# Performance work log

Measured on AMD Instinct MI355X. Metric: run time of the kernel, lower is better.

The kernel has to match this reference:

```python
import jax, jax.numpy as jnp
import numpy as np

N_NODES = 100000
N_EDGES = 1250000
HID = 64
IN_CH = 64
OUT_CH = 16
N_GRAPHS = 512


def setup_inputs() -> dict:
    key = jax.random.key(0)
    ks = jax.random.split(key, 20)
    x = jax.random.normal(ks[0], (N_NODES, IN_CH), dtype=jnp.float32)
    edge_index = jax.random.randint(ks[1], (2, N_EDGES), 0, N_NODES, dtype=jnp.int64)
    batch = jnp.sort(jax.random.randint(ks[2], (N_NODES,), 0, N_GRAPHS, dtype=jnp.int64))
    s_in = 1.0 / np.sqrt(IN_CH)
    s_h = 1.0 / np.sqrt(HID)
    u = lambda k, shp, s: jax.random.uniform(k, shp, jnp.float32, -s, s)
    return {
        "x": x, "edge_index": edge_index, "batch": batch,
        "W0": u(ks[3], (IN_CH, HID), s_in), "b0": u(ks[4], (HID,), s_in),
        "W1a": u(ks[5], (HID, HID), s_h), "b1a": u(ks[6], (HID,), s_h),
        "W1b": u(ks[7], (HID, HID), s_h), "b1b": u(ks[8], (HID,), s_h),
        "W2a": u(ks[9], (HID, HID), s_h), "b2a": u(ks[10], (HID,), s_h),
        "W2b": u(ks[11], (HID, HID), s_h), "b2b": u(ks[12], (HID,), s_h),
        "W3a": u(ks[13], (HID, HID), s_h), "b3a": u(ks[14], (HID,), s_h),
        "W3b": u(ks[15], (HID, HID), s_h), "b3b": u(ks[16], (HID,), s_h),
        "Wl": u(ks[17], (HID, OUT_CH), s_h), "bl": u(ks[18], (OUT_CH,), s_h),
    }


def _gin_conv(h, src, dst, Wa, ba, Wb, bb):
    # GINConv, eps=0: mlp(x_i + sum_{j->i} x_j); mlp = Linear,ReLU,Linear
    agg = jax.ops.segment_sum(h[src], dst, num_segments=N_NODES)  # [N, HID]
    z = h + agg
    return jax.nn.relu(z @ Wa + ba) @ Wb + bb


def reference(x, edge_index, batch, W0, b0, W1a, b1a, W1b, b1b,
              W2a, b2a, W2b, b2b, W3a, b3a, W3b, b3b, Wl, bl):
    src, dst = edge_index[0], edge_index[1]
    h = jax.nn.relu(x @ W0 + b0)
    h = jax.nn.relu(_gin_conv(h, src, dst, W1a, b1a, W1b, b1b))
    h = jax.nn.relu(_gin_conv(h, src, dst, W2a, b2a, W2b, b2b))
    h = jax.nn.relu(_gin_conv(h, src, dst, W3a, b3a, W3b, b3b))
    # global mean pool over graphs
    sums = jax.ops.segment_sum(h, batch, num_segments=N_GRAPHS)  # [G, HID]
    cnts = jax.ops.segment_sum(jnp.ones((N_NODES,), h.dtype), batch, num_segments=N_GRAPHS)
    pooled = sums / jnp.maximum(cnts, 1.0)[:, None]
    # dropout p=0.5 is identity in eval mode
    return pooled @ Wl + bl  # [G, OUT_CH]
```

## Files before the change

### kernel.cpp

```cpp
#include <hip/hip_runtime.h>
#include <hip/hip_fp16.h>

#define N_NODES 100000
#define N_EDGES 1250000
#define HID 64
#define N_GRAPHS 512
#define OUT_CH 16

#define NSUP 196
#define SB_CAP 8192
#define E_BLK 2048
#define NPB ((N_EDGES + E_BLK - 1) / E_BLK)
#define TILE2 ((N_NODES + 127) / 128)
#define NWP 6
#define TSTRIDE 68
#define AGG_BLOCKS 3125

typedef _Float16 h16;
typedef _Float16 half2_t __attribute__((ext_vector_type(2)));
typedef _Float16 f16x8 __attribute__((ext_vector_type(8)));
typedef float f32x4 __attribute__((ext_vector_type(4)));

__device__ __forceinline__ void acc4(uint2 u, float& a0, float& a1, float& a2, float& a3) {
    half2_t h0 = __builtin_bit_cast(half2_t, u.x);
    half2_t h1 = __builtin_bit_cast(half2_t, u.y);
    a0 += (float)h0[0];
    a1 += (float)h0[1];
    a2 += (float)h1[0];
    a3 += (float)h1[1];
}

__device__ __forceinline__ void acc8(uint4 u, float* a) {
    half2_t h0 = __builtin_bit_cast(half2_t, u.x);
    half2_t h1 = __builtin_bit_cast(half2_t, u.y);
    half2_t h2 = __builtin_bit_cast(half2_t, u.z);
    half2_t h3 = __builtin_bit_cast(half2_t, u.w);
    a[0] += (float)h0[0]; a[1] += (float)h0[1];
    a[2] += (float)h1[0]; a[3] += (float)h1[1];
    a[4] += (float)h2[0]; a[5] += (float)h2[1];
    a[6] += (float)h3[0]; a[7] += (float)h3[1];
}

__device__ __forceinline__ unsigned pack2(float x, float y) {
    half2_t o;
    o[0] = (h16)x;
    o[1] = (h16)y;
    return __builtin_bit_cast(unsigned, o);
}

__global__ __launch_bounds__(256) void k_fat(const int* __restrict__ src,
                                             const int* __restrict__ dst,
                                             int* __restrict__ cnt,
                                             int* __restrict__ buckets,
                                             const float* __restrict__ W1a,
                                             const float* __restrict__ W1b,
                                             const float* __restrict__ W2a,
                                             const float* __restrict__ W2b,
                                             const float* __restrict__ W3a,
                                             const float* __restrict__ W3b,
                                             h16* __restrict__ WF,
                                             const float* __restrict__ W0,
                                             const float* __restrict__ B0,
                                             const float* __restrict__ Xin,
                                             h16* __restrict__ Hout) {
    __shared__ int hist[256];
    __shared__ int gbase[256];
    __shared__ int tsum[256];
    __shared__ __align__(16) int stage[E_BLK];
    __shared__ __align__(16) float sT[4 * 16 * TSTRIDE];

    int b = blockIdx.x;
    int t = threadIdx.x;

    if (b < NPB) {
        int e0 = b * E_BLK;
        int eN = N_EDGES - e0;
        if (eN > E_BLK) eN = E_BLK;

        hist[t] = 0;
        __syncthreads();
        for (int i = t; i < eN; i += 256) atomicAdd(&hist[dst[e0 + i] >> 9], 1);
        __syncthreads();

        int c = hist[t];
        tsum[t] = c;
        __syncthreads();
        for (int off = 1; off < 256; off <<= 1) {
            int u = (t >= off) ? tsum[t - off] : 0;
            __syncthreads();
            tsum[t] += u;
            __syncthreads();
        }
        int pref = tsum[t] - c;
        if (t < NSUP && c > 0) gbase[t] = atomicAdd(&cnt[t], c);
        hist[t] = pref;
        __syncthreads();

        for (int i = t; i < eN; i += 256) {
            int s = src[e0 + i];
            int d = dst[e0 + i];
            int p = atomicAdd(&hist[d >> 9], 1);
            stage[p] = ((d & 511) << 17) | s;
        }
        __syncthreads();

        if (t < NSUP && c > 0) {
            int lstart = hist[t] - c;
            int gb = gbase[t];
            int cap = SB_CAP - gb;
            int n = c < cap ? c : (cap > 0 ? cap : 0);
            int* dp = buckets + (size_t)t * SB_CAP + gb;
            int r = 0;
            while (r < n && (((size_t)(dp + r)) & 15)) { dp[r] = stage[lstart + r]; ++r; }
            for (; r + 4 <= n; r += 4) {
                int4 v;
                v.x = stage[lstart + r];
                v.y = stage[lstart + r + 1];
                v.z = stage[lstart + r + 2];
                v.w = stage[lstart + r + 3];
                *(int4*)(dp + r) = v;
            }
            for (; r < n; ++r) dp[r] = stage[lstart + r];
        }
    } else if (b < NPB + NWP) {
        const float* Ws[NWP] = {W1a, W1b, W2a, W2b, W3a, W3b};
        const float* W = Ws[b - NPB];
        h16* dstW = WF + (size_t)(b - NPB) * 4096;
#pragma unroll
        for (int i = 0; i < 16; ++i) {
            int s = t + 256 * i;
            int k = s >> 6, col = s & 63;
            int kc = k >> 5, quad = (k >> 3) & 3, j = k & 7;
            int c = col >> 4, n = col & 15;
            dstW[((c * 2 + kc) * 4 + quad) * 128 + n * 8 + j] = (h16)W[s];
        }
    } else {
        int lb = b - NPB - NWP;
        int w = t >> 6, lane = t & 63;
        int n16 = lane & 15, quad = lane >> 4;
        float* T = sT + w * 16 * TSTRIDE;

        f16x8 bw[4][2];
#pragma unroll
        for (int c = 0; c < 4; ++c)
#pragma unroll
            for (int kc = 0; kc < 2; ++kc) {
                f16x8 v;
#pragma unroll
                for (int j = 0; j < 8; ++j)
                    v[j] = (h16)W0[(kc * 32 + quad * 8 + j) * 64 + c * 16 + n16];
                bw[c][kc] = v;
            }
        float bv[4];
#pragma unroll
        for (int c = 0; c < 4; ++c) bv[c] = B0[c * 16 + n16];

#pragma unroll
        for (int tt = 0; tt < 2; ++tt) {
            int rbase = lb * 128 + tt * 64 + w * 16;
            int arow = rbase + n16;
            int crow = arow < N_NODES ? arow : N_NODES - 1;
            f16x8 a[2];
#pragma unroll
            for (int kc = 0; kc < 2; ++kc) {
                const float4* xp = (const float4*)(Xin + (size_t)crow * HID + kc * 32 + quad * 8);
                float4 p = xp[0], q = xp[1];
                f16x8 v;
                v[0] = (h16)p.x; v[1] = (h16)p.y; v[2] = (h16)p.z; v[3] = (h16)p.w;
                v[4] = (h16)q.x; v[5] = (h16)q.y; v[6] = (h16)q.z; v[7] = (h16)q.w;
                a[kc] = v;
            }

            f32x4 acc[4];
#pragma unroll
            for (int c = 0; c < 4; ++c) {
                acc[c] = (f32x4){bv[c], bv[c], bv[c], bv[c]};
#pragma unroll
                for (int kc = 0; kc < 2; ++kc)
                    acc[c] = __builtin_amdgcn_mfma_f32_16x16x32_f16(a[kc], bw[c][kc], acc[c], 0, 0, 0);
            }

#pragma unroll
            for (int c = 0; c < 4; ++c)
#pragma unroll
                for (int r = 0; r < 4; ++r)
                    T[(quad * 4 + r) * TSTRIDE + c * 16 + n16] = fmaxf(acc[c][r], 0.f);
            {
                int rl = lane >> 2, seg = lane & 3;
                int row = rbase + rl;
                if (row < N_NODES) {
                    const float* tr = &T[rl * TSTRIDE + seg * 16];
                    f16x8 o0, o1;
#pragma unroll
                    for (int i = 0; i < 8; ++i) {
                        o0[i] = (h16)tr[i];
                        o1[i] = (h16)tr[8 + i];
                    }
                    f16x8* dp = (f16x8*)(Hout + (size_t)row * HID + seg * 16);
                    dp[0] = o0;
                    dp[1] = o1;
                }
            }
        }
    }
}

__global__ __launch_bounds__(256) void k_sort(const int* __restrict__ cnt,
                                              int* __restrict__ buckets,
                                              int* __restrict__ rowptrS) {
    __shared__ int srt[SB_CAP];
    __shared__ int hist[512];
    __shared__ int curs[512];
    __shared__ int tsum[256];
    int s = blockIdx.x, t = threadIdx.x;
    int n = cnt[s];
    n = n < SB_CAP ? n : SB_CAP;
    int* gb = buckets + (size_t)s * SB_CAP;
    int sBase = s * SB_CAP;

    hist[t] = 0;
    hist[t + 256] = 0;
    __syncthreads();
    for (int i = t; i < n; i += 256) atomicAdd(&hist[gb[i] >> 17], 1);
    __syncthreads();

    int c0 = hist[2 * t], c1 = hist[2 * t + 1];
    int tot = c0 + c1;
    tsum[t] = tot;
    __syncthreads();
    for (int off = 1; off < 256; off <<= 1) {
        int u = (t >= off) ? tsum[t - off] : 0;
        __syncthreads();
        tsum[t] += u;
        __syncthreads();
    }
    int pref = tsum[t] - tot;
    curs[2 * t] = pref;
    curs[2 * t + 1] = pref + c0;
    rowptrS[s * 513 + 2 * t] = sBase + pref;
    rowptrS[s * 513 + 2 * t + 1] = sBase + pref + c0;
    if (t == 255) rowptrS[s * 513 + 512] = sBase + n;
    __syncthreads();

    for (int i = t; i < n; i += 256) {
        int rec = gb[i];
        int pos = atomicAdd(&curs[rec >> 17], 1);
        srt[pos] = rec;
    }
    __syncthreads();
    for (int i = t; i < n; i += 256) gb[i] = srt[i];
}

__global__ __launch_bounds__(256) void k_aggregate(const int* __restrict__ rowptrS,
                                                   const int* __restrict__ buckets,
                                                   const h16* __restrict__ H,
                                                   h16* __restrict__ Z) {
    const uint4* H8 = (const uint4*)H;
    uint4* Z8 = (uint4*)Z;
    int lane = threadIdx.x & 63;
    int part = lane >> 3, sub = lane & 7;
    int gwave = (blockIdx.x * 256 + threadIdx.x) >> 6;
    int nw = (gridDim.x * 256) >> 6;
    for (int i0 = gwave * 8; i0 < N_NODES; i0 += nw * 8) {
        int i = i0 + part;
        bool valid = i < N_NODES;
        int iv = valid ? i : N_NODES - 1;
        int s = iv >> 9, l = iv & 511;
        int start = rowptrS[s * 513 + l];
        int end = valid ? rowptrS[s * 513 + l + 1] : start;
        float a[8] = {0.f, 0.f, 0.f, 0.f, 0.f, 0.f, 0.f, 0.f};
        acc8(H8[(size_t)iv * 8 + sub], a);
        int j = start;
        for (; j + 8 <= end; j += 8) {
            int s0 = buckets[j] & 0x1FFFF;
            int s1 = buckets[j + 1] & 0x1FFFF;
            int s2 = buckets[j + 2] & 0x1FFFF;
            int s3 = buckets[j + 3] & 0x1FFFF;
            int s4 = buckets[j + 4] & 0x1FFFF;
            int s5 = buckets[j + 5] & 0x1FFFF;
            int s6 = buckets[j + 6] & 0x1FFFF;
            int s7 = buckets[j + 7] & 0x1FFFF;
            uint4 u0 = H8[(size_t)s0 * 8 + sub];
            uint4 u1 = H8[(size_t)s1 * 8 + sub];
            uint4 u2 = H8[(size_t)s2 * 8 + sub];
            uint4 u3 = H8[(size_t)s3 * 8 + sub];
            uint4 u4 = H8[(size_t)s4 * 8 + sub];
            uint4 u5 = H8[(size_t)s5 * 8 + sub];
            uint4 u6 = H8[(size_t)s6 * 8 + sub];
            uint4 u7 = H8[(size_t)s7 * 8 + sub];
            acc8(u0, a);
            acc8(u1, a);
            acc8(u2, a);
            acc8(u3, a);
            acc8(u4, a);
            acc8(u5, a);
            acc8(u6, a);
            acc8(u7, a);
        }
        if (j + 4 <= end) {
            int s0 = buckets[j] & 0x1FFFF;
            int s1 = buckets[j + 1] & 0x1FFFF;
            int s2 = buckets[j + 2] & 0x1FFFF;
            int s3 = buckets[j + 3] & 0x1FFFF;
            uint4 u0 = H8[(size_t)s0 * 8 + sub];
            uint4 u1 = H8[(size_t)s1 * 8 + sub];
            uint4 u2 = H8[(size_t)s2 * 8 + sub];
            uint4 u3 = H8[(size_t)s3 * 8 + sub];
            acc8(u0, a);
            acc8(u1, a);
            acc8(u2, a);
            acc8(u3, a);
            j += 4;
        }
        if (j + 2 <= end) {
            int s0 = buckets[j] & 0x1FFFF;
            int s1 = buckets[j + 1] & 0x1FFFF;
            uint4 u0 = H8[(size_t)s0 * 8 + sub];
            uint4 u1 = H8[(size_t)s1 * 8 + sub];
            acc8(u0, a);
            acc8(u1, a);
            j += 2;
        }
        if (j < end) {
            int s0 = buckets[j] & 0x1FFFF;
            acc8(H8[(size_t)s0 * 8 + sub], a);
        }
        if (valid) {
            uint4 o;
            o.x = pack2(a[0], a[1]);
            o.y = pack2(a[2], a[3]);
            o.z = pack2(a[4], a[5]);
            o.w = pack2(a[6], a[7]);
            Z8[(size_t)i * 8 + sub] = o;
        }
    }
}

__global__ __launch_bounds__(256) void k_mlp(const h16* __restrict__ WaF,
                                             const float* __restrict__ Ba,
                                             const h16* __restrict__ WbF,
                                             const float* __restrict__ Bb,
                                             const h16* __restrict__ Zin,
                                             h16* __restrict__ Hout) {
    __shared__ __align__(16) float sT[4 * 16 * TSTRIDE];
    int t = threadIdx.x;
    int w = t >> 6, lane = t & 63;
    int n16 = lane & 15, quad = lane >> 4;
    float* T = sT + w * 16 * TSTRIDE;

    f16x8 bwa[4][2], bwb[4][2];
#pragma unroll
    for (int c = 0; c < 4; ++c)
#pragma unroll
        for (int kc = 0; kc < 2; ++kc) {
            int f = ((c * 2 + kc) * 4 + quad) * 128 + n16 * 8;
            bwa[c][kc] = *(const f16x8*)(WaF + f);
            bwb[c][kc] = *(const f16x8*)(WbF + f);
        }
    float bva[4], bvb[4];
#pragma unroll
    for (int c = 0; c < 4; ++c) {
        bva[c] = Ba[c * 16 + n16];
        bvb[c] = Bb[c * 16 + n16];
    }

#pragma unroll
    for (int tt = 0; tt < 2; ++tt) {
        int rbase = blockIdx.x * 128 + tt * 64 + w * 16;
        int arow = rbase + n16;
        int crow = arow < N_NODES ? arow : N_NODES - 1;
        const f16x8* zp = (const f16x8*)(Zin + (size_t)crow * HID + quad * 8);
        f16x8 a0 = zp[0];
        f16x8 a1 = zp[4];

        f32x4 acc[4];
#pragma unroll
        for (int c = 0; c < 4; ++c) {
            acc[c] = (f32x4){bva[c], bva[c], bva[c], bva[c]};
            acc[c] = __builtin_amdgcn_mfma_f32_16x16x32_f16(a0, bwa[c][0], acc[c], 0, 0, 0);
            acc[c] = __builtin_amdgcn_mfma_f32_16x16x32_f16(a1, bwa[c][1], acc[c], 0, 0, 0);
        }

#pragma unroll
        for (int c = 0; c < 4; ++c)
#pragma unroll
            for (int r = 0; r < 4; ++r)
                T[(quad * 4 + r) * TSTRIDE + c * 16 + n16] = fmaxf(acc[c][r], 0.f);

        f16x8 ta[2];
#pragma unroll
        for (int kc = 0; kc < 2; ++kc) {
            float4 p = *(const float4*)&T[n16 * TSTRIDE + kc * 32 + quad * 8];
            float4 q = *(const float4*)&T[n16 * TSTRIDE + kc * 32 + quad * 8 + 4];
            f16x8 v;
            v[0] = (h16)p.x; v[1] = (h16)p.y; v[2] = (h16)p.z; v[3] = (h16)p.w;
            v[4] = (h16)q.x; v[5] = (h16)q.y; v[6] = (h16)q.z; v[7] = (h16)q.w;
            ta[kc] = v;
        }

#pragma unroll
        for (int c = 0; c < 4; ++c) {
            acc[c] = (f32x4){bvb[c], bvb[c], bvb[c], bvb[c]};
            acc[c] = __builtin_amdgcn_mfma_f32_16x16x32_f16(ta[0], bwb[c][0], acc[c], 0, 0, 0);
            acc[c] = __builtin_amdgcn_mfma_f32_16x16x32_f16(ta[1], bwb[c][1], acc[c], 0, 0, 0);
        }

#pragma unroll
        for (int c = 0; c < 4; ++c)
#pragma unroll
            for (int r = 0; r < 4; ++r)
                T[(quad * 4 + r) * TSTRIDE + c * 16 + n16] = fmaxf(acc[c][r], 0.f);
        {
            int rl = lane >> 2, seg = lane & 3;
            int row = rbase + rl;
            if (row < N_NODES) {
                const float* tr = &T[rl * TSTRIDE + seg * 16];
                f16x8 o0, o1;
#pragma unroll
                for (int i = 0; i < 8; ++i) {
                    o0[i] = (h16)tr[i];
                    o1[i] = (h16)tr[8 + i];
                }
                f16x8* dp = (f16x8*)(Hout + (size_t)row * HID + seg * 16);
                dp[0] = o0;
                dp[1] = o1;
            }
        }
    }
}

__global__ __launch_bounds__(256) void k_poolfinal(const h16* __restrict__ H,
                                                   const int* __restrict__ batch,
                                                   const float* __restrict__ Wl,
                                                   const float* __restrict__ bl,
                                                   float* __restrict__ out) {
    __shared__ float sp[4 * HID];
    int g = blockIdx.x;
    int t = threadIdx.x;
    int lane = t & 63, w = t >> 6;
    int lo = 0, hi = N_NODES;
    while (lo < hi) { int m = (lo + hi) >> 1; if (batch[m] < g) lo = m + 1; else hi = m; }
    int start = lo;
    hi = N_NODES;
    while (lo < hi) { int m = (lo + hi) >> 1; if (batch[m] < g + 1) lo = m + 1; else hi = m; }
    int end = lo;
    float s0 = 0.f, s1 = 0.f, s2 = 0.f, s3 = 0.f;
    int r = start + w;
    for (; r + 12 < end; r += 16) {
        float v0 = (float)H[(size_t)r * HID + lane];
        float v1 = (float)H[(size_t)(r + 4) * HID + lane];
        float v2 = (float)H[(size_t)(r + 8) * HID + lane];
        float v3 = (float)H[(size_t)(r + 12) * HID + lane];
        s0 += v0; s1 += v1; s2 += v2; s3 += v3;
    }
    for (; r < end; r += 4) s0 += (float)H[(size_t)r * HID + lane];
    sp[w * HID + lane] = s0 + s1 + s2 + s3;
    __syncthreads();
    if (t < HID) {
        float tot = sp[t] + sp[HID + t] + sp[2 * HID + t] + sp[3 * HID + t];
        float c = (end > start) ? (float)(end - start) : 1.0f;
        sp[t] = tot / c;
    }
    __syncthreads();
    if (t < OUT_CH) {
        float acc = bl[t];
#pragma unroll
        for (int k = 0; k < HID; ++k) acc += sp[k] * Wl[k * OUT_CH + t];
        out[g * OUT_CH + t] = acc;
    }
}

extern "C" void kernel_launch(void* const* d_in, const int* in_sizes, int n_in,
                              void* d_out, int out_size, void* d_ws, size_t ws_size,
                              hipStream_t stream) {
    const float* x     = (const float*)d_in[0];
    const int*   edge  = (const int*)d_in[1];
    const int*   batch = (const int*)d_in[2];
    const float* W0  = (const float*)d_in[3];
    const float* b0  = (const float*)d_in[4];
    const float* W1a = (const float*)d_in[5];
    const float* b1a = (const float*)d_in[6];
    const float* W1b = (const float*)d_in[7];
    const float* b1b = (const float*)d_in[8];
    const float* W2a = (const float*)d_in[9];
    const float* b2a = (const float*)d_in[10];
    const float* W2b = (const float*)d_in[11];
    const float* b2b = (const float*)d_in[12];
    const float* W3a = (const float*)d_in[13];
    const float* b3a = (const float*)d_in[14];
    const float* W3b = (const float*)d_in[15];
    const float* b3b = (const float*)d_in[16];
    const float* Wl  = (const float*)d_in[17];
    const float* bl  = (const float*)d_in[18];
    float* out = (float*)d_out;

    const int* src = edge;
    const int* dst = edge + N_EDGES;

    h16* HA = (h16*)d_ws;
    h16* Z  = HA + (size_t)N_NODES * HID;
    int* cnt     = (int*)(Z + (size_t)N_NODES * HID);
    int* rowptrS = cnt + NSUP;
    int* buckets = rowptrS + NSUP * 513;
    h16* WF      = (h16*)(buckets + (size_t)NSUP * SB_CAP);
    h16* W1aF = WF;
    h16* W1bF = WF + 4096 * 1;
    h16* W2aF = WF + 4096 * 2;
    h16* W2bF = WF + 4096 * 3;
    h16* W3aF = WF + 4096 * 4;
    h16* W3bF = WF + 4096 * 5;

    hipMemsetAsync(cnt, 0, NSUP * sizeof(int), stream);
    k_fat<<<NPB + NWP + TILE2, 256, 0, stream>>>(src, dst, cnt, buckets,
        W1a, W1b, W2a, W2b, W3a, W3b, WF, W0, b0, x, HA);
    k_sort<<<NSUP, 256, 0, stream>>>(cnt, buckets, rowptrS);

    k_aggregate<<<AGG_BLOCKS, 256, 0, stream>>>(rowptrS, buckets, HA, Z);
    k_mlp<<<TILE2, 256, 0, stream>>>(W1aF, b1a, W1bF, b1b, Z, HA);

    k_aggregate<<<AGG_BLOCKS, 256, 0, stream>>>(rowptrS, buckets, HA, Z);
    k_mlp<<<TILE2, 256, 0, stream>>>(W2aF, b2a, W2bF, b2b, Z, HA);

    k_aggregate<<<AGG_BLOCKS, 256, 0, stream>>>(rowptrS, buckets, HA, Z);
    k_mlp<<<TILE2, 256, 0, stream>>>(W3aF, b3a, W3bF, b3b, Z, HA);

    k_poolfinal<<<N_GRAPHS, 256, 0, stream>>>(HA, batch, Wl, bl, out);
}
```

Measured before the change: 273.4 us.

## Move input linear into sort kernel and prefetch first 16 neighbor indices

The first-layer linear transform (x@W0+b0, ReLU) moves out of the edge-partition kernel and into the bucket-sort kernel. Sort blocks and linear-transform blocks now share one launch and use a union shared-memory buffer. This rebalances the two pre-processing launches and keeps the sort's large shared array from sitting alongside the partition kernel's buffers. The aggregation loop now loads the first 16 neighbor indices up front with clamped addresses and issues predicated gathers in two batches of 8. This aims to cut dependent-latency chains for typical degrees, at the cost of extra register use and redundant index loads for low-degree nodes.

```diff
diff --git a/kernel.cpp b/kernel.cpp
--- a/kernel.cpp
+++ b/kernel.cpp
@@ -15,20 +15,12 @@
 #define NWP 6
 #define TSTRIDE 68
 #define AGG_BLOCKS 3125
+#define SMEM_UNION 37888
 
 typedef _Float16 h16;
 typedef _Float16 half2_t __attribute__((ext_vector_type(2)));
 typedef _Float16 f16x8 __attribute__((ext_vector_type(8)));
 typedef float f32x4 __attribute__((ext_vector_type(4)));
-
-__device__ __forceinline__ void acc4(uint2 u, float& a0, float& a1, float& a2, float& a3) {
-    half2_t h0 = __builtin_bit_cast(half2_t, u.x);
-    half2_t h1 = __builtin_bit_cast(half2_t, u.y);
-    a0 += (float)h0[0];
-    a1 += (float)h0[1];
-    a2 += (float)h1[0];
-    a3 += (float)h1[1];
-}
 
 __device__ __forceinline__ void acc8(uint4 u, float* a) {
     half2_t h0 = __builtin_bit_cast(half2_t, u.x);
@@ -48,26 +40,21 @@
     return __builtin_bit_cast(unsigned, o);
 }
 
-__global__ __launch_bounds__(256) void k_fat(const int* __restrict__ src,
-                                             const int* __restrict__ dst,
-                                             int* __restrict__ cnt,
-                                             int* __restrict__ buckets,
-                                             const float* __restrict__ W1a,
-                                             const float* __restrict__ W1b,
-                                             const float* __restrict__ W2a,
-                                             const float* __restrict__ W2b,
-                                             const float* __restrict__ W3a,
-                                             const float* __restrict__ W3b,
-                                             h16* __restrict__ WF,
-                                             const float* __restrict__ W0,
-                                             const float* __restrict__ B0,
-                                             const float* __restrict__ Xin,
-                                             h16* __restrict__ Hout) {
+__global__ __launch_bounds__(256) void k_part(const int* __restrict__ src,
+                                              const int* __restrict__ dst,
+                                              int* __restrict__ cnt,
+                                              int* __restrict__ buckets,
+                                              const float* __restrict__ W1a,
+                                              const float* __restrict__ W1b,
+                                              const float* __restrict__ W2a,
+                                              const float* __restrict__ W2b,
+                                              const float* __restrict__ W3a,
+                                              const float* __restrict__ W3b,
+                                              h16* __restrict__ WF) {
     __shared__ int hist[256];
     __shared__ int gbase[256];
     __shared__ int tsum[256];
     __shared__ __align__(16) int stage[E_BLK];
-    __shared__ __align__(16) float sT[4 * 16 * TSTRIDE];
 
     int b = blockIdx.x;
     int t = threadIdx.x;
@@ -122,7 +109,7 @@
             }
             for (; r < n; ++r) dp[r] = stage[lstart + r];
         }
-    } else if (b < NPB + NWP) {
+    } else {
         const float* Ws[NWP] = {W1a, W1b, W2a, W2b, W3a, W3b};
         const float* W = Ws[b - NPB];
         h16* dstW = WF + (size_t)(b - NPB) * 4096;
@@ -134,8 +121,65 @@
             int c = col >> 4, n = col & 15;
             dstW[((c * 2 + kc) * 4 + quad) * 128 + n * 8 + j] = (h16)W[s];
         }
+    }
+}
+
+__global__ __launch_bounds__(256) void k_sortlin(const int* __restrict__ cnt,
+                                                 int* __restrict__ buckets,
+                                                 int* __restrict__ rowptrS,
+                                                 const float* __restrict__ W0,
+                                                 const float* __restrict__ B0,
+                                                 const float* __restrict__ Xin,
+                                                 h16* __restrict__ Hout) {
+    __shared__ __align__(16) char smem[SMEM_UNION];
+    int b = blockIdx.x;
+    int t = threadIdx.x;
+
+    if (b < NSUP) {
+        int* srt  = (int*)smem;
+        int* hist = (int*)(smem + 32768);
+        int* curs = (int*)(smem + 34816);
+        int* tsum = (int*)(smem + 36864);
+        int s = b;
+        int n = cnt[s];
+        n = n < SB_CAP ? n : SB_CAP;
+        int* gb = buckets + (size_t)s * SB_CAP;
+        int sBase = s * SB_CAP;
+
+        hist[t] = 0;
+        hist[t + 256] = 0;
+        __syncthreads();
+        for (int i = t; i < n; i += 256) atomicAdd(&hist[gb[i] >> 17], 1);
+        __syncthreads();
+
+        int c0 = hist[2 * t], c1 = hist[2 * t + 1];
+        int tot = c0 + c1;
+        tsum[t] = tot;
+        __syncthreads();
+        for (int off = 1; off < 256; off <<= 1) {
+            int u = (t >= off) ? tsum[t - off] : 0;
+            __syncthreads();
+            tsum[t] += u;
+            __syncthreads();
+        }
+        int pref = tsum[t] - tot;
+        curs[2 * t] = pref;
+        curs[2 * t + 1] = pref + c0;
+        rowptrS[s * 513 + 2 * t] = sBase + pref;
+        rowptrS[s * 513 + 2 * t + 1] = sBase + pref + c0;
+        if (t == 255) rowptrS[s * 513 + 512] = sBase + n;
+        __syncthreads();
+
+        for (int i = t; i < n; i += 256) {
+            int rec = gb[i];
+            int pos = atomicAdd(&curs[rec >> 17], 1);
+            srt[pos] = rec;
+        }
+        __syncthreads();
+        for (int i = t; i < n; i += 256) gb[i] = srt[i];
     } else {
-        int lb = b - NPB - NWP;
+        float* sT = (float*)smem;
+        int lb = b - NSUP;
         int w = t >> 6, lane = t & 63;
         int n16 = lane & 15, quad = lane >> 4;
         float* T = sT + w * 16 * TSTRIDE;
@@ -201,54 +245,9 @@
                     dp[1] = o1;
                 }
             }
-        }
-    }
-}
-
-__global__ __launch_bounds__(256) void k_sort(const int* __restrict__ cnt,
-                                              int* __restrict__ buckets,
-                                              int* __restrict__ rowptrS) {
-    __shared__ int srt[SB_CAP];
-    __shared__ int hist[512];
-    __shared__ int curs[512];
-    __shared__ int tsum[256];
-    int s = blockIdx.x, t = threadIdx.x;
-    int n = cnt[s];
-    n = n < SB_CAP ? n : SB_CAP;
-    int* gb = buckets + (size_t)s * SB_CAP;
-    int sBase = s * SB_CAP;
-
-    hist[t] = 0;
-    hist[t + 256] = 0;
-    __syncthreads();
-    for (int i = t; i < n; i += 256) atomicAdd(&hist[gb[i] >> 17], 1);
-    __syncthreads();
-
-    int c0 = hist[2 * t], c1 = hist[2 * t + 1];
-    int tot = c0 + c1;
-    tsum[t] = tot;
-    __syncthreads();
-    for (int off = 1; off < 256; off <<= 1) {
-        int u = (t >= off) ? tsum[t - off] : 0;
-        __syncthreads();
-        tsum[t] += u;
-        __syncthreads();
-    }
-    int pref = tsum[t] - tot;
-    curs[2 * t] = pref;
-    curs[2 * t + 1] = pref + c0;
-    rowptrS[s * 513 + 2 * t] = sBase + pref;
-    rowptrS[s * 513 + 2 * t + 1] = sBase + pref + c0;
-    if (t == 255) rowptrS[s * 513 + 512] = sBase + n;
-    __syncthreads();
-
-    for (int i = t; i < n; i += 256) {
-        int rec = gb[i];
-        int pos = atomicAdd(&curs[rec >> 17], 1);
-        srt[pos] = rec;
-    }
-    __syncthreads();
-    for (int i = t; i < n; i += 256) gb[i] = srt[i];
+            __syncthreads();
+        }
+    }
 }
 
 __global__ __launch_bounds__(256) void k_aggregate(const int* __restrict__ rowptrS,
@@ -270,60 +269,77 @@
         int end = valid ? rowptrS[s * 513 + l + 1] : start;
         float a[8] = {0.f, 0.f, 0.f, 0.f, 0.f, 0.f, 0.f, 0.f};
         acc8(H8[(size_t)iv * 8 + sub], a);
-        int j = start;
-        for (; j + 8 <= end; j += 8) {
-            int s0 = buckets[j] & 0x1FFFF;
-            int s1 = buckets[j + 1] & 0x1FFFF;
-            int s2 = buckets[j + 2] & 0x1FFFF;
-            int s3 = buckets[j + 3] & 0x1FFFF;
-            int s4 = buckets[j + 4] & 0x1FFFF;
-            int s5 = buckets[j + 5] & 0x1FFFF;
-            int s6 = buckets[j + 6] & 0x1FFFF;
-            int s7 = buckets[j + 7] & 0x1FFFF;
-            uint4 u0 = H8[(size_t)s0 * 8 + sub];
-            uint4 u1 = H8[(size_t)s1 * 8 + sub];
-            uint4 u2 = H8[(size_t)s2 * 8 + sub];
-            uint4 u3 = H8[(size_t)s3 * 8 + sub];
-            uint4 u4 = H8[(size_t)s4 * 8 + sub];
-            uint4 u5 = H8[(size_t)s5 * 8 + sub];
-            uint4 u6 = H8[(size_t)s6 * 8 + sub];
-            uint4 u7 = H8[(size_t)s7 * 8 + sub];
-            acc8(u0, a);
-            acc8(u1, a);
-            acc8(u2, a);
-            acc8(u3, a);
-            acc8(u4, a);
-            acc8(u5, a);
-            acc8(u6, a);
-            acc8(u7, a);
-        }
-        if (j + 4 <= end) {
-            int s0 = buckets[j] & 0x1FFFF;
-            int s1 = buckets[j + 1] & 0x1FFFF;
-            int s2 = buckets[j + 2] & 0x1FFFF;
-            int s3 = buckets[j + 3] & 0x1FFFF;
-            uint4 u0 = H8[(size_t)s0 * 8 + sub];
-            uint4 u1 = H8[(size_t)s1 * 8 + sub];
-            uint4 u2 = H8[(size_t)s2 * 8 + sub];
-            uint4 u3 = H8[(size_t)s3 * 8 + sub];
-            acc8(u0, a);
-            acc8(u1, a);
-            acc8(u2, a);
-            acc8(u3, a);
-            j += 4;
-        }
-        if (j + 2 <= end) {
-            int s0 = buckets[j] & 0x1FFFF;
-            int s1 = buckets[j + 1] & 0x1FFFF;
-            uint4 u0 = H8[(size_t)s0 * 8 + sub];
-            uint4 u1 = H8[(size_t)s1 * 8 + sub];
-            acc8(u0, a);
-            acc8(u1, a);
-            j += 2;
-        }
-        if (j < end) {
-            int s0 = buckets[j] & 0x1FFFF;
-            acc8(H8[(size_t)s0 * 8 + sub], a);
+        int deg = end - start;
+        if (deg > 0) {
+            int last = end - 1;
+            int ix[16];
+#pragma unroll
+            for (int k = 0; k < 16; ++k) {
+                int p = start + k;
+                ix[k] = buckets[p < last ? p : last] & 0x1FFFF;
+            }
+            uint4 u[8];
+#pragma unroll
+            for (int k = 0; k < 8; ++k)
+                if (deg > k) u[k] = H8[(size_t)ix[k] * 8 + sub];
+#pragma unroll
+            for (int k = 0; k < 8; ++k)
+                if (deg > k) acc8(u[k], a);
+            if (deg > 8) {
+#pragma unroll
+                for (int k = 0; k < 8; ++k)
+                    if (deg > 8 + k) u[k] = H8[(size_t)ix[8 + k] * 8 + sub];
+#pragma unroll
+                for (int k = 0; k < 8; ++k)
+                    if (deg > 8 + k) acc8(u[k], a);
+            }
+            if (deg > 16) {
+                int j = start + 16;
+                for (; j + 8 <= end; j += 8) {
+                    int s0 = buckets[j] & 0x1FFFF;
+                    int s1 = buckets[j + 1] & 0x1FFFF;
+                    int s2 = buckets[j + 2] & 0x1FFFF;
+                    int s3 = buckets[j + 3] & 0x1FFFF;
+                    int s4 = buckets[j + 4] & 0x1FFFF;
+                    int s5 = buckets[j + 5] & 0x1FFFF;
+                    int s6 = buckets[j + 6] & 0x1FFFF;
+                    int s7 = buckets[j + 7] & 0x1FFFF;
+                    uint4 v0 = H8[(size_t)s0 * 8 + sub];
+                    uint4 v1 = H8[(size_t)s1 * 8 + sub];
+                    uint4 v2 = H8[(size_t)s2 * 8 + sub];
+                    uint4 v3 = H8[(size_t)s3 * 8 + sub];
+                    uint4 v4 = H8[(size_t)s4 * 8 + sub];
+                    uint4 v5 = H8[(size_t)s5 * 8 + sub];
+                    uint4 v6 = H8[(size_t)s6 * 8 + sub];
+                    uint4 v7 = H8[(size_t)s7 * 8 + sub];
+                    acc8(v0, a); acc8(v1, a); acc8(v2, a); acc8(v3, a);
+                    acc8(v4, a); acc8(v5, a); acc8(v6, a); acc8(v7, a);
+                }
+                if (j + 4 <= end) {
+                    int s0 = buckets[j] & 0x1FFFF;
+                    int s1 = buckets[j + 1] & 0x1FFFF;
+                    int s2 = buckets[j + 2] & 0x1FFFF;
+                    int s3 = buckets[j + 3] & 0x1FFFF;
+                    uint4 v0 = H8[(size_t)s0 * 8 + sub];
+                    uint4 v1 = H8[(size_t)s1 * 8 + sub];
+                    uint4 v2 = H8[(size_t)s2 * 8 + sub];
+                    uint4 v3 = H8[(size_t)s3 * 8 + sub];
+                    acc8(v0, a); acc8(v1, a); acc8(v2, a); acc8(v3, a);
+                    j += 4;
+                }
+                if (j + 2 <= end) {
+                    int s0 = buckets[j] & 0x1FFFF;
+                    int s1 = buckets[j + 1] & 0x1FFFF;
+                    uint4 v0 = H8[(size_t)s0 * 8 + sub];
+                    uint4 v1 = H8[(size_t)s1 * 8 + sub];
+                    acc8(v0, a); acc8(v1, a);
+                    j += 2;
+                }
+                if (j < end) {
+                    int s0 = buckets[j] & 0x1FFFF;
+                    acc8(H8[(size_t)s0 * 8 + sub], a);
+                }
+            }
         }
         if (valid) {
             uint4 o;
@@ -511,9 +527,9 @@
     h16* W3bF = WF + 4096 * 5;
 
     hipMemsetAsync(cnt, 0, NSUP * sizeof(int), stream);
-    k_fat<<<NPB + NWP + TILE2, 256, 0, stream>>>(src, dst, cnt, buckets,
-        W1a, W1b, W2a, W2b, W3a, W3b, WF, W0, b0, x, HA);
-    k_sort<<<NSUP, 256, 0, stream>>>(cnt, buckets, rowptrS);
+    k_part<<<NPB + NWP, 256, 0, stream>>>(src, dst, cnt, buckets,
+        W1a, W1b, W2a, W2b, W3a, W3b, WF);
+    k_sortlin<<<NSUP + TILE2, 256, 0, stream>>>(cnt, buckets, rowptrS, W0, b0, x, HA);
 
     k_aggregate<<<AGG_BLOCKS, 256, 0, stream>>>(rowptrS, buckets, HA, Z);
     k_mlp<<<TILE2, 256, 0, stream>>>(W1aF, b1a, W1bF, b1b, Z, HA);
```

After: 274.8 us. About the same (+0.5%).
